# Kernel optimization log

Hardware: AMD Instinct MI355X
Metric: run time of the kernel (lower is better)

## Reference

```python
import jax, jax.numpy as jnp
import numpy as np

T = 2048          # total (flattened) tokens
HID = 4096
NQ = 32           # query heads
NKV = 8           # kv heads
D = 128           # head_dim
B = 4             # dllm block length (block-sparse attention block)
WIN = 1024        # sliding window
EPS = 1e-6


def _rope_tables():
    # standard RoPE cos/sin tables, half-dim frequencies duplicated
    inv_freq = 1.0 / (10000.0 ** (np.arange(0, D, 2, dtype=np.float32) / D))
    pos = np.arange(T, dtype=np.float32)
    freqs = np.outer(pos, inv_freq)                     # [T, D/2]
    emb = np.concatenate([freqs, freqs], axis=-1)       # [T, D]
    return jnp.asarray(np.cos(emb)), jnp.asarray(np.sin(emb))


def setup_inputs() -> dict:
    key = jax.random.key(0)
    ks = jax.random.split(key, 4)
    cos, sin = _rope_tables()
    return {
        "hidden_states": jax.random.normal(ks[0], (T, HID), jnp.float32),
        "cos": cos,
        "sin": sin,
        "w_qkv": jax.random.normal(ks[1], (HID, (NQ + 2 * NKV) * D), jnp.float32) * (HID ** -0.5),
        "q_norm_w": jnp.ones((D,), jnp.float32),
        "k_norm_w": jnp.ones((D,), jnp.float32),
        "w_o": jax.random.normal(ks[2], (NQ * D, HID), jnp.float32) * ((NQ * D) ** -0.5),
    }


def _rmsnorm(x, w):
    # per-head RMSNorm over last dim (head_dim)
    var = jnp.mean(jnp.square(x), axis=-1, keepdims=True)
    return x * jax.lax.rsqrt(var + EPS) * w


def _rotate_half(x):
    x1, x2 = jnp.split(x, 2, axis=-1)
    return jnp.concatenate([-x2, x1], axis=-1)


def reference(hidden_states, cos, sin, w_qkv, q_norm_w, k_norm_w, w_o):
    # fused QKV projection on flattened tokens [T, HID]
    qkv = hidden_states @ w_qkv                                  # [T, (NQ+2NKV)*D]
    q, k, v = jnp.split(qkv, [NQ * D, (NQ + NKV) * D], axis=-1)
    q = q.reshape(T, NQ, D)
    k = k.reshape(T, NKV, D)
    v = v.reshape(T, NKV, D)

    # per-head QK RMSNorm
    q = _rmsnorm(q, q_norm_w)
    k = _rmsnorm(k, k_norm_w)

    # RoPE
    c = cos[:, None, :]
    s = sin[:, None, :]
    q = q * c + _rotate_half(q) * s
    k = k * c + _rotate_half(k) * s

    # GQA: expand kv heads to query heads
    groups = NQ // NKV
    k = jnp.repeat(k, groups, axis=1)                            # [T, NQ, D]
    v = jnp.repeat(v, groups, axis=1)

    # block-sparse (dLLM block-causal) + sliding-window mask:
    # token q attends to token j iff block(j) <= block(q) (full bidirectional
    # attention within a dllm block, causal across blocks) AND j is within
    # the sliding window.
    pos = jnp.arange(T)
    qb = pos // B
    allowed = (qb[None, :] <= qb[:, None]) & ((pos[:, None] - pos[None, :]) < WIN)

    scale = D ** -0.5
    scores = jnp.einsum("qhd,khd->hqk", q, k) * scale            # [NQ, T, T]
    scores = jnp.where(allowed[None, :, :], scores, jnp.float32(-1e30))
    probs = jax.nn.softmax(scores, axis=-1)
    attn = jnp.einsum("hqk,khd->qhd", probs, v)                   # [T, NQ, D]

    out = attn.reshape(T, NQ * D) @ w_o                           # [T, HID]
    return out
```

## Files before the change

kernel.cpp:

```cpp
#include <hip/hip_runtime.h>
#include <hip/hip_bf16.h>

typedef unsigned short u16;
typedef __attribute__((ext_vector_type(8))) short bf16x8;
typedef __attribute__((ext_vector_type(4))) float f32x4;
typedef __attribute__((ext_vector_type(8))) u16 u16x8;
typedef __attribute__((ext_vector_type(4))) u16 u16x4;

#define T_SEQ 2048
#define HID 4096
#define NQ 32
#define NKV 8
#define DH 128
#define WIN 1024

__device__ __forceinline__ u16 f2bf(float f) {
  union { float f; unsigned int u; } v; v.f = f;
  unsigned int u = v.u;
  unsigned int r = (u + 0x7FFFu + ((u >> 16) & 1u)) >> 16;
  return (u16)r;
}
__device__ __forceinline__ float bf2f(u16 b) {
  union { unsigned int u; float f; } v; v.u = ((unsigned int)b) << 16;
  return v.f;
}

__device__ __forceinline__ void gload16(const void* g, void* l) {
  __builtin_amdgcn_global_load_lds(
      (const __attribute__((address_space(1))) unsigned int*)g,
      (__attribute__((address_space(3))) unsigned int*)l, 16, 0, 0);
}

__global__ __launch_bounds__(256) void f32_to_bf16(const float* __restrict__ in,
                                                   u16* __restrict__ out, int n) {
  int i = (blockIdx.x * 256 + threadIdx.x) * 8;
  if (i >= n) return;
  float4 a = *(const float4*)(in + i);
  float4 b = *(const float4*)(in + i + 4);
  u16x8 r;
  r[0] = f2bf(a.x); r[1] = f2bf(a.y); r[2] = f2bf(a.z); r[3] = f2bf(a.w);
  r[4] = f2bf(b.x); r[5] = f2bf(b.y); r[6] = f2bf(b.z); r[7] = f2bf(b.w);
  *(u16x8*)(out + i) = r;
}

__global__ __launch_bounds__(256) void transpose_f32_to_bf16(const float* __restrict__ in,
                                                             u16* __restrict__ out,
                                                             int R, int C) {
  __shared__ float tile[64][65];
  int c0 = blockIdx.x * 64, r0 = blockIdx.y * 64;
  int tx = threadIdx.x, ty = threadIdx.y;
#pragma unroll
  for (int i = 0; i < 64; i += 16) {
    float4 v = *(const float4*)(in + (size_t)(r0 + ty + i) * C + c0 + tx * 4);
    tile[ty + i][tx * 4 + 0] = v.x;
    tile[ty + i][tx * 4 + 1] = v.y;
    tile[ty + i][tx * 4 + 2] = v.z;
    tile[ty + i][tx * 4 + 3] = v.w;
  }
  __syncthreads();
#pragma unroll
  for (int i = 0; i < 64; i += 16) {
    u16x4 o;
#pragma unroll
    for (int j = 0; j < 4; ++j) o[j] = f2bf(tile[tx * 4 + j][ty + i]);
    *(u16x4*)(out + (size_t)(c0 + ty + i) * R + r0 + tx * 4) = o;
  }
}

template <int NF, bool BF16OUT>
__global__ __launch_bounds__(512, 2) void gemm_2w(const u16* __restrict__ A,
                                                  const u16* __restrict__ Bt,
                                                  void* __restrict__ Cv,
                                                  int N, int K, int NT) {
  constexpr int HN = NF * 16;
  constexpr int BN = 4 * HN;
  constexpr int NB = BN / 64;
  __shared__ u16 lsA[2][16384];
  __shared__ u16 lsB[2][BN * 64];
  const int tid = threadIdx.x;
  const int lane = tid & 63, w = tid >> 6;
  const int wm = w >> 1, wn = w & 1;
  const int l15 = lane & 15, l4 = lane >> 4;

  const int nwg = gridDim.x;
  const int cpx = nwg >> 3;
  const int bid = blockIdx.x;
  const int swz = (bid & 7) * cpx + (bid >> 3);
  const int bm = (swz & 7) * 256;
  const int bn = (swz >> 3) * BN;

  auto stageA = [&](int unit, int slot, int kt) {
    int r = tid >> 3, cp = tid & 7;
    int scp = cp ^ (r & 7);
    gload16(A + (size_t)(bm + unit * 64 + r) * K + kt * 64 + scp * 8,
            (char*)lsA[slot] + (unit * 512 + tid) * 16);
  };
  auto stageB = [&](int unit, int slot, int kt) {
    int r = tid >> 3, cp = tid & 7;
    int scp = cp ^ (r & 7);
    gload16(Bt + (size_t)(bn + unit * 64 + r) * K + kt * 64 + scp * 8,
            (char*)lsB[slot] + (unit * 512 + tid) * 16);
  };
  auto rdA = [&](int slot, int mh, int mf, int ks) -> bf16x8 {
    int r = wm * 64 + mh * 32 + mf * 16 + l15;
    int ch = (ks * 4 + l4) ^ (r & 7);
    return *(const bf16x8*)(lsA[slot] + r * 64 + ch * 8);
  };
  auto rdB = [&](int slot, int nh, int nf, int ks) -> bf16x8 {
    int r = wn * 2 * HN + nh * HN + nf * 16 + l15;
    int ch = (ks * 4 + l4) ^ (r & 7);
    return *(const bf16x8*)(lsB[slot] + r * 64 + ch * 8);
  };

#define WAIT_NB() do { if constexpr (NB == 3) asm volatile("s_waitcnt vmcnt(3)" ::: "memory"); \
                       else                   asm volatile("s_waitcnt vmcnt(2)" ::: "memory"); } while (0)

  f32x4 acc[4][2 * NF] = {};
  bf16x8 afA[2][2], afB[2][2], bfr[2 * NF][2];

  stageA(0, 0, 0); stageA(1, 0, 0); stageA(2, 0, 0); stageA(3, 0, 0);
#pragma unroll
  for (int u = 0; u < NB; ++u) stageB(u, 0, 0);
#pragma unroll
  for (int u = 0; u < NB; ++u) stageB(u, 1, 1);
  WAIT_NB();
  __builtin_amdgcn_s_barrier();

  for (int t = 0; t < NT; ++t) {
    const int s = t & 1;
    const int ktA = (t + 1 < NT) ? t + 1 : NT - 1;
    const int ktB = (t + 2 < NT) ? t + 2 : NT - 1;

#pragma unroll
    for (int mf = 0; mf < 2; ++mf)
#pragma unroll
      for (int ks = 0; ks < 2; ++ks) afA[mf][ks] = rdA(s, 0, mf, ks);
#pragma unroll
    for (int nf = 0; nf < NF; ++nf)
#pragma unroll
      for (int ks = 0; ks < 2; ++ks) {
        bfr[nf][ks] = rdB(s, 0, nf, ks);
        bfr[NF + nf][ks] = rdB(s, 1, nf, ks);
      }
    stageA(0, s ^ 1, ktA); stageA(1, s ^ 1, ktA);
    stageA(2, s ^ 1, ktA); stageA(3, s ^ 1, ktA);
    __builtin_amdgcn_s_barrier();
    asm volatile("s_waitcnt lgkmcnt(0)" ::: "memory");
    __builtin_amdgcn_sched_barrier(0);
    __builtin_amdgcn_s_setprio(1);
#pragma unroll
    for (int mf = 0; mf < 2; ++mf)
#pragma unroll
      for (int nf = 0; nf < 2 * NF; ++nf) {
        acc[mf][nf] = __builtin_amdgcn_mfma_f32_16x16x32_bf16(afA[mf][0], bfr[nf][0], acc[mf][nf], 0, 0, 0);
        acc[mf][nf] = __builtin_amdgcn_mfma_f32_16x16x32_bf16(afA[mf][1], bfr[nf][1], acc[mf][nf], 0, 0, 0);
      }
    __builtin_amdgcn_s_setprio(0);
    __builtin_amdgcn_s_barrier();

#pragma unroll
    for (int mf = 0; mf < 2; ++mf)
#pragma unroll
      for (int ks = 0; ks < 2; ++ks) afB[mf][ks] = rdA(s, 1, mf, ks);
#pragma unroll
    for (int u = 0; u < NB; ++u) stageB(u, s, ktB);
    __builtin_amdgcn_s_barrier();
    asm volatile("s_waitcnt lgkmcnt(0)" ::: "memory");
    __builtin_amdgcn_sched_barrier(0);
    __builtin_amdgcn_s_setprio(1);
#pragma unroll
    for (int mf = 0; mf < 2; ++mf)
#pragma unroll
      for (int nf = 0; nf < 2 * NF; ++nf) {
        acc[2 + mf][nf] = __builtin_amdgcn_mfma_f32_16x16x32_bf16(afB[mf][0], bfr[nf][0], acc[2 + mf][nf], 0, 0, 0);
        acc[2 + mf][nf] = __builtin_amdgcn_mfma_f32_16x16x32_bf16(afB[mf][1], bfr[nf][1], acc[2 + mf][nf], 0, 0, 0);
      }
    __builtin_amdgcn_s_setprio(0);
    WAIT_NB();
    __builtin_amdgcn_s_barrier();
  }

  asm volatile("s_waitcnt vmcnt(0)" ::: "memory");

#pragma unroll
  for (int mi = 0; mi < 4; ++mi)
#pragma unroll
    for (int ni = 0; ni < 2 * NF; ++ni) {
      int row = bm + wm * 64 + mi * 16 + l4 * 4;
      int col = bn + wn * 2 * HN + ni * 16 + l15;
      if constexpr (BF16OUT) {
        u16* dst = (u16*)Cv;
#pragma unroll
        for (int j = 0; j < 4; ++j)
          dst[(size_t)(row + j) * N + col] = f2bf(acc[mi][ni][j]);
      } else {
        float* p = (float*)Cv + (size_t)row * N + col;
        p[0] = acc[mi][ni][0];
        p[(size_t)N] = acc[mi][ni][1];
        p[2 * (size_t)N] = acc[mi][ni][2];
        p[3 * (size_t)N] = acc[mi][ni][3];
      }
    }
#undef WAIT_NB
}

__global__ __launch_bounds__(256) void rope_kernel(const u16* __restrict__ qkv,
                                                   const float* __restrict__ cosb,
                                                   const float* __restrict__ sinb,
                                                   const float* __restrict__ qw,
                                                   const float* __restrict__ kw,
                                                   u16* __restrict__ Qo,
                                                   u16* __restrict__ Ko,
                                                   u16* __restrict__ Vt) {
  int wid = threadIdx.x >> 6, lane = threadIdx.x & 63;
  int item = blockIdx.x * 4 + wid;
  int t = item / 48, hid = item % 48;
  const u16* x = qkv + (size_t)t * 6144 + hid * 128;
  float x1 = bf2f(x[lane]), x2 = bf2f(x[lane + 64]);
  if (hid < NQ + NKV) {
    float ss = x1 * x1 + x2 * x2;
    for (int off = 32; off; off >>= 1) ss += __shfl_xor(ss, off);
    float inv = rsqrtf(ss * (1.0f / 128.0f) + 1e-6f);
    const float* wn = (hid < NQ) ? qw : kw;
    float n1 = x1 * inv * wn[lane], n2 = x2 * inv * wn[lane + 64];
    float c1 = cosb[t * 128 + lane], s1 = sinb[t * 128 + lane];
    float c2 = cosb[t * 128 + lane + 64], s2 = sinb[t * 128 + lane + 64];
    float o1 = n1 * c1 - n2 * s1;
    float o2 = n2 * c2 + n1 * s2;
    if (hid < NQ) {
      const float scale = 0.08838834764831845f;
      u16* q = Qo + ((size_t)hid * T_SEQ + t) * 128;
      q[lane] = f2bf(o1 * scale); q[lane + 64] = f2bf(o2 * scale);
    } else {
      int h = hid - NQ;
      u16* k = Ko + ((size_t)h * T_SEQ + t) * 128;
      k[lane] = f2bf(o1); k[lane + 64] = f2bf(o2);
    }
  } else {
    int h = hid - (NQ + NKV);
    Vt[((size_t)h * 128 + lane) * T_SEQ + t] = x[lane];
    Vt[((size_t)h * 128 + lane + 64) * T_SEQ + t] = x[lane + 64];
  }
}

__global__ __launch_bounds__(256) void attn_kernel(const u16* __restrict__ Q,
                                                   const u16* __restrict__ Kb,
                                                   const u16* __restrict__ Vt,
                                                   u16* __restrict__ O) {
  __shared__ u16 kls[2][64 * 128];
  __shared__ u16 vls[2][128 * 64];
  __shared__ u16 plds[4][16 * 72];

  const int tid = threadIdx.x;
  const int lane = tid & 63, w = tid >> 6;
  const int l15 = lane & 15, l4 = lane >> 4;
  const int h = blockIdx.x;
  const int q0 = blockIdx.y * 64;
  const int wq0 = q0 + w * 16;
  const int kvh = h >> 2;

  bf16x8 qf[4];
  {
    const u16* qrow = Q + ((size_t)h * T_SEQ + (wq0 + l15)) * DH;
    for (int ks = 0; ks < 4; ++ks)
      qf[ks] = *(const bf16x8*)(qrow + ks * 32 + l4 * 8);
  }

  f32x4 acc[8] = {};
  float m = -1e30f, lsum = 0.f;

  int ks0 = q0 - (WIN - 1); if (ks0 < 0) ks0 = 0;
  ks0 &= ~63;
  const int kend = q0;

  auto stage = [&](int b, int k0) {
#pragma unroll
    for (int c = 0; c < 4; ++c) {
      int base = w * 4096 + c * 1024;
      int idx = base / 16 + lane;
      {
        int row = idx >> 4;
        int col = (idx & 15) ^ (row & 7);
        gload16(Kb + ((size_t)kvh * T_SEQ + k0 + row) * DH + col * 8,
                (char*)kls[b] + base);
      }
      {
        int d = idx >> 3;
        int ch = (idx & 7) ^ (d & 7);
        gload16(Vt + ((size_t)kvh * DH + d) * T_SEQ + k0 + ch * 8,
                (char*)vls[b] + base);
      }
    }
  };

  stage(0, ks0);
  int buf = 0;
  for (int k0 = ks0; k0 <= kend; k0 += 64) {
    bool more = (k0 + 64 <= kend);
    if (more) stage(buf ^ 1, k0 + 64);
    if (more) { asm volatile("s_waitcnt vmcnt(8)" ::: "memory"); }
    else      { asm volatile("s_waitcnt vmcnt(0)" ::: "memory"); }
    __builtin_amdgcn_s_barrier();
    __builtin_amdgcn_sched_barrier(0);

    if (k0 <= wq0 + 15 && k0 + 63 >= wq0 - (WIN - 1)) {
      f32x4 st[4];
      __builtin_amdgcn_s_setprio(1);
#pragma unroll
      for (int kh = 0; kh < 4; ++kh) {
        f32x4 s = {};
        int row = kh * 16 + l15;
        const char* kb = (const char*)kls[buf] + row * 256;
#pragma unroll
        for (int ks = 0; ks < 4; ++ks) {
          int chunk = (ks * 4 + l4) ^ (row & 7);
          bf16x8 kf = *(const bf16x8*)(kb + chunk * 16);
          s = __builtin_amdgcn_mfma_f32_16x16x32_bf16(kf, qf[ks], s, 0, 0, 0);
        }
        st[kh] = s;
      }
      __builtin_amdgcn_s_setprio(0);
      const int q = wq0 + l15;
      float pv[4][4];
      float mx = -3e38f;
      if (k0 + 64 <= wq0 && k0 >= wq0 - 1008) {
#pragma unroll
        for (int kh = 0; kh < 4; ++kh)
#pragma unroll
          for (int i = 0; i < 4; ++i) {
            pv[kh][i] = st[kh][i];
            mx = fmaxf(mx, pv[kh][i]);
          }
      } else {
#pragma unroll
        for (int kh = 0; kh < 4; ++kh)
#pragma unroll
          for (int i = 0; i < 4; ++i) {
            int k = k0 + kh * 16 + l4 * 4 + i;
            bool ok = ((k >> 2) <= (q >> 2)) && (q - k < WIN);
            float s = ok ? st[kh][i] : -3e38f;
            pv[kh][i] = s;
            mx = fmaxf(mx, s);
          }
      }
      mx = fmaxf(mx, __shfl_xor(mx, 16));
      mx = fmaxf(mx, __shfl_xor(mx, 32));
      if (!__all(mx <= m + 8.f)) {
        float mn = fmaxf(m, mx);
        float sc = __expf(m - mn);
        m = mn;
        lsum *= sc;
#pragma unroll
        for (int nt = 0; nt < 8; ++nt)
#pragma unroll
          for (int i = 0; i < 4; ++i) acc[nt][i] *= sc;
      }
      float rs = 0.f;
#pragma unroll
      for (int kh = 0; kh < 4; ++kh)
#pragma unroll
        for (int i = 0; i < 4; ++i) {
          float p = __expf(pv[kh][i] - m);
          pv[kh][i] = p;
          rs += p;
        }
      rs += __shfl_xor(rs, 16);
      rs += __shfl_xor(rs, 32);
      lsum += rs;
      u16* pw = plds[w];
#pragma unroll
      for (int kh = 0; kh < 4; ++kh) {
        unsigned int d0 = (unsigned int)f2bf(pv[kh][0]) | ((unsigned int)f2bf(pv[kh][1]) << 16);
        unsigned int d1 = (unsigned int)f2bf(pv[kh][2]) | ((unsigned int)f2bf(pv[kh][3]) << 16);
        *(unsigned int*)(pw + l15 * 72 + kh * 16 + l4 * 4) = d0;
        *(unsigned int*)(pw + l15 * 72 + kh * 16 + l4 * 4 + 2) = d1;
      }
      bf16x8 pf0 = *(const bf16x8*)(pw + l15 * 72 + l4 * 8);
      bf16x8 pf1 = *(const bf16x8*)(pw + l15 * 72 + 32 + l4 * 8);
      __builtin_amdgcn_s_setprio(1);
#pragma unroll
      for (int nt = 0; nt < 8; ++nt) {
        int d = nt * 16 + l15;
        int ch0 = l4 ^ (d & 7);
        int ch1 = (4 + l4) ^ (d & 7);
        bf16x8 vf0 = *(const bf16x8*)((const char*)vls[buf] + d * 128 + ch0 * 16);
        bf16x8 vf1 = *(const bf16x8*)((const char*)vls[buf] + d * 128 + ch1 * 16);
        acc[nt] = __builtin_amdgcn_mfma_f32_16x16x32_bf16(vf0, pf0, acc[nt], 0, 0, 0);
        acc[nt] = __builtin_amdgcn_mfma_f32_16x16x32_bf16(vf1, pf1, acc[nt], 0, 0, 0);
      }
      __builtin_amdgcn_s_setprio(0);
    }
    __builtin_amdgcn_sched_barrier(0);
    __builtin_amdgcn_s_barrier();
    buf ^= 1;
  }

  float inv = 1.0f / lsum;
#pragma unroll
  for (int nt = 0; nt < 8; ++nt) {
    u16x4 o;
#pragma unroll
    for (int i = 0; i < 4; ++i) o[i] = f2bf(acc[nt][i] * inv);
    *(u16x4*)(O + (size_t)(wq0 + l15) * (NQ * DH) + h * DH + nt * 16 + l4 * 4) = o;
  }
}

extern "C" void kernel_launch(void* const* d_in, const int* in_sizes, int n_in,
                              void* d_out, int out_size, void* d_ws, size_t ws_size,
                              hipStream_t stream) {
  const float* hidden = (const float*)d_in[0];
  const float* cosb   = (const float*)d_in[1];
  const float* sinb   = (const float*)d_in[2];
  const float* w_qkv  = (const float*)d_in[3];
  const float* qnw    = (const float*)d_in[4];
  const float* knw    = (const float*)d_in[5];
  const float* w_o    = (const float*)d_in[6];
  float* out = (float*)d_out;
  char* ws = (char*)d_ws;

  u16*   wqkvT  = (u16*)(ws);
  u16*   hid_bf = (u16*)(ws + ((size_t)48 << 20));
  u16*   qkv_bf = (u16*)(ws + ((size_t)64 << 20));
  u16*   q_bf   = (u16*)(ws + ((size_t)112 << 20));
  u16*   k_bf   = (u16*)(ws + ((size_t)128 << 20));
  u16*   vt_bf  = (u16*)(ws + ((size_t)132 << 20));
  u16*   attn_bf= (u16*)(ws + ((size_t)48 << 20));
  u16*   woT    = (u16*)(ws);

  f32_to_bf16<<<4096, 256, 0, stream>>>(hidden, hid_bf, T_SEQ * HID);
  transpose_f32_to_bf16<<<dim3(96, 64), dim3(16, 16), 0, stream>>>(w_qkv, wqkvT, HID, 6144);
  gemm_2w<3, true><<<256, 512, 0, stream>>>(hid_bf, wqkvT, qkv_bf, 6144, HID, 64);
  transpose_f32_to_bf16<<<dim3(64, 64), dim3(16, 16), 0, stream>>>(w_o, woT, NQ * DH, HID);
  rope_kernel<<<(T_SEQ * 48) / 4, 256, 0, stream>>>(qkv_bf, cosb, sinb, qnw, knw, q_bf, k_bf, vt_bf);
  attn_kernel<<<dim3(NQ, T_SEQ / 64), 256, 0, stream>>>(q_bf, k_bf, vt_bf, attn_bf);
  gemm_2w<2, false><<<256, 512, 0, stream>>>(attn_bf, woT, out, HID, NQ * DH, 64);
}
```

Before: 319.9 us.

## Add software-pipelined output-projection GEMM with triple-buffered A and swizzled LDS

Replaces the generic output-projection GEMM with a dedicated kernel that triple-buffers A tiles and double-buffers B tiles in LDS, using XOR-swizzled layouts and explicit waitcnt/barrier placement. Each k-tile is split into two half-phases so register fragment loads for the next step overlap the current MFMA work, with s_setprio raising priority during MFMA bursts. It also remaps workgroup IDs for L2 locality. The hand-scheduled synchronization adds complexity and risks LDS pressure limiting occupancy.

```diff
diff --git a/kernel.cpp b/kernel.cpp
--- a/kernel.cpp
+++ b/kernel.cpp
@@ -202,6 +202,138 @@
       }
     }
 #undef WAIT_NB
+}
+
+#define MFMA16(a, b, c) __builtin_amdgcn_mfma_f32_16x16x32_bf16(a, b, c, 0, 0, 0)
+__global__ __launch_bounds__(512, 2) void gemm2_p(const u16* __restrict__ A,
+                                                  const u16* __restrict__ Bt,
+                                                  float* __restrict__ C,
+                                                  int N, int K, int NT) {
+  __shared__ u16 lsA[3][16384];
+  __shared__ u16 lsB[2][8192];
+  const int tid = threadIdx.x;
+  const int lane = tid & 63, w = tid >> 6;
+  const int wm = w >> 1, wn = w & 1;
+  const int l15 = lane & 15, l4 = lane >> 4;
+
+  const int nwg = gridDim.x;
+  const int cpx = nwg >> 3;
+  const int bid = blockIdx.x;
+  const int swz = (bid & 7) * cpx + (bid >> 3);
+  const int bm = (swz & 7) * 256;
+  const int bn = (swz >> 3) * 128;
+
+  auto stageA = [&](int unit, int slot, int kt) {
+    int r = tid >> 3, cp = tid & 7;
+    int scp = cp ^ (r & 7);
+    gload16(A + (size_t)(bm + unit * 64 + r) * K + kt * 64 + scp * 8,
+            (char*)lsA[slot] + (unit * 512 + tid) * 16);
+  };
+  auto stageB = [&](int unit, int slot, int kt) {
+    int r = tid >> 3, cp = tid & 7;
+    int scp = cp ^ (r & 7);
+    gload16(Bt + (size_t)(bn + unit * 64 + r) * K + kt * 64 + scp * 8,
+            (char*)lsB[slot] + (unit * 512 + tid) * 16);
+  };
+  auto rdA = [&](int slot, int mfi, int ks) -> bf16x8 {
+    int r = wm * 64 + mfi * 16 + l15;
+    int ch = (ks * 4 + l4) ^ (r & 7);
+    return *(const bf16x8*)(lsA[slot] + r * 64 + ch * 8);
+  };
+  auto rdB = [&](int slot, int nf, int ks) -> bf16x8 {
+    int r = wn * 64 + nf * 16 + l15;
+    int ch = (ks * 4 + l4) ^ (r & 7);
+    return *(const bf16x8*)(lsB[slot] + r * 64 + ch * 8);
+  };
+
+  f32x4 acc[4][4] = {};
+  bf16x8 afA0[4], afA1[4], bfr0_[8], bfr1_[8], afB[4];
+
+  stageA(0, 0, 0); stageA(1, 0, 0); stageA(2, 0, 0); stageA(3, 0, 0);
+  stageB(0, 0, 0); stageB(1, 0, 0);
+  stageA(0, 1, 1); stageA(1, 1, 1); stageA(2, 1, 1); stageA(3, 1, 1);
+  stageB(0, 1, 1); stageB(1, 1, 1);
+  asm volatile("s_waitcnt vmcnt(6)" ::: "memory");
+  __builtin_amdgcn_s_barrier();
+#pragma unroll
+  for (int mf = 0; mf < 2; ++mf)
+#pragma unroll
+    for (int ks = 0; ks < 2; ++ks) afA0[mf * 2 + ks] = rdA(0, mf, ks);
+#pragma unroll
+  for (int nf = 0; nf < 4; ++nf)
+#pragma unroll
+    for (int ks = 0; ks < 2; ++ks) bfr0_[nf * 2 + ks] = rdB(0, nf, ks);
+  asm volatile("s_waitcnt lgkmcnt(0)" ::: "memory");
+  __builtin_amdgcn_sched_barrier(0);
+
+#define TILE_P(T, AFC, BFC, AFN, BFN) {                                        \
+    const int s3 = (T) % 3, s3n = ((T) + 1) % 3, s3s = ((T) + 2) % 3;          \
+    const int s2 = (T) & 1, s2n = ((T) + 1) & 1;                               \
+    const int ktt = ((T) + 2 < NT) ? (T) + 2 : NT - 1;                         \
+                                                             \
+    stageA(0, s3s, ktt); stageA(1, s3s, ktt);                                  \
+    stageA(2, s3s, ktt); stageA(3, s3s, ktt);                                  \
+    asm volatile("s_waitcnt vmcnt(4)" ::: "memory");                           \
+    _Pragma("unroll")                                                          \
+    for (int mf = 0; mf < 2; ++mf)                                             \
+      _Pragma("unroll")                                                        \
+      for (int ks = 0; ks < 2; ++ks) afB[mf * 2 + ks] = rdA(s3, 2 + mf, ks);   \
+    _Pragma("unroll")                                                          \
+    for (int nf = 0; nf < 4; ++nf)                                             \
+      _Pragma("unroll")                                                        \
+      for (int ks = 0; ks < 2; ++ks) BFN[nf * 2 + ks] = rdB(s2n, nf, ks);      \
+    __builtin_amdgcn_s_setprio(1);                                             \
+    _Pragma("unroll")                                                          \
+    for (int mf = 0; mf < 2; ++mf)                                             \
+      _Pragma("unroll")                                                        \
+      for (int nf = 0; nf < 4; ++nf) {                                         \
+        acc[mf][nf] = MFMA16(AFC[mf * 2 + 0], BFC[nf * 2 + 0], acc[mf][nf]);   \
+        acc[mf][nf] = MFMA16(AFC[mf * 2 + 1], BFC[nf * 2 + 1], acc[mf][nf]);   \
+      }                                                                        \
+    __builtin_amdgcn_s_setprio(0);                                             \
+    asm volatile("s_waitcnt lgkmcnt(0)" ::: "memory");                         \
+    __builtin_amdgcn_sched_barrier(0);                                         \
+    __builtin_amdgcn_s_barrier();                                              \
+                                                             \
+    _Pragma("unroll")                                                          \
+    for (int mf = 0; mf < 2; ++mf)                                             \
+      _Pragma("unroll")                                                        \
+      for (int ks = 0; ks < 2; ++ks) AFN[mf * 2 + ks] = rdA(s3n, mf, ks);      \
+    stageB(0, s2, ktt); stageB(1, s2, ktt);                                    \
+    __builtin_amdgcn_s_setprio(1);                                             \
+    _Pragma("unroll")                                                          \
+    for (int mf = 0; mf < 2; ++mf)                                             \
+      _Pragma("unroll")                                                        \
+      for (int nf = 0; nf < 4; ++nf) {                                         \
+        acc[2 + mf][nf] = MFMA16(afB[mf * 2 + 0], BFC[nf * 2 + 0], acc[2 + mf][nf]); \
+        acc[2 + mf][nf] = MFMA16(afB[mf * 2 + 1], BFC[nf * 2 + 1], acc[2 + mf][nf]); \
+      }                                                                        \
+    __builtin_amdgcn_s_setprio(0);                                             \
+    asm volatile("s_waitcnt lgkmcnt(0)" ::: "memory");                         \
+    __builtin_amdgcn_sched_barrier(0);                                         \
+    __builtin_amdgcn_s_barrier();                                              \
+  }
+
+  for (int t = 0; t < NT; t += 2) {
+    TILE_P(t, afA0, bfr0_, afA1, bfr1_);
+    TILE_P(t + 1, afA1, bfr1_, afA0, bfr0_);
+  }
+#undef TILE_P
+
+  asm volatile("s_waitcnt vmcnt(0)" ::: "memory");
+
+#pragma unroll
+  for (int mi = 0; mi < 4; ++mi)
+#pragma unroll
+    for (int ni = 0; ni < 4; ++ni) {
+      int row = bm + wm * 64 + mi * 16 + l4 * 4;
+      int col = bn + wn * 64 + ni * 16 + l15;
+      float* p = C + (size_t)row * N + col;
+      p[0] = acc[mi][ni][0];
+      p[(size_t)N] = acc[mi][ni][1];
+      p[2 * (size_t)N] = acc[mi][ni][2];
+      p[3 * (size_t)N] = acc[mi][ni][3];
+    }
 }
 
 __global__ __launch_bounds__(256) void rope_kernel(const u16* __restrict__ qkv,
@@ -433,5 +565,5 @@
   transpose_f32_to_bf16<<<dim3(64, 64), dim3(16, 16), 0, stream>>>(w_o, woT, NQ * DH, HID);
   rope_kernel<<<(T_SEQ * 48) / 4, 256, 0, stream>>>(qkv_bf, cosb, sinb, qnw, knw, q_bf, k_bf, vt_bf);
   attn_kernel<<<dim3(NQ, T_SEQ / 64), 256, 0, stream>>>(q_bf, k_bf, vt_bf, attn_bf);
-  gemm_2w<2, false><<<256, 512, 0, stream>>>(attn_bf, woT, out, HID, NQ * DH, 64);
-}
+  gemm2_p<<<256, 512, 0, stream>>>(attn_bf, woT, out, HID, NQ * DH, 64);
+}
```

New measurement: 330.7 us. 3.4% more time.

## Add triple-buffered A-tile GEMM variant for QKV projection

Applied to the files above, without the earlier changes.

Adds a gemm_3s kernel that keeps three LDS slots for the A tile (B stays double-buffered) and prefetches two k-steps ahead, splitting each iteration into two MFMA halves with staged loads between them. It is used for the QKV projection GEMM in place of gemm_2w. The aim is to hide more global-load latency behind the matrix math. In exchange it uses more shared memory, which may limit occupancy at 2 workgroups per CU, and its vmcnt accounting is hand-tuned.

```diff
diff --git a/kernel.cpp b/kernel.cpp
--- a/kernel.cpp
+++ b/kernel.cpp
@@ -65,6 +65,145 @@
     for (int j = 0; j < 4; ++j) o[j] = f2bf(tile[tx * 4 + j][ty + i]);
     *(u16x4*)(out + (size_t)(c0 + ty + i) * R + r0 + tx * 4) = o;
   }
+}
+
+template <int NF, bool BF16OUT>
+__global__ __launch_bounds__(512, 2) void gemm_3s(const u16* __restrict__ A,
+                                                  const u16* __restrict__ Bt,
+                                                  void* __restrict__ Cv,
+                                                  int N, int K, int NT) {
+  constexpr int HN = NF * 16;
+  constexpr int BN = 4 * HN;
+  constexpr int NB = BN / 64;
+  __shared__ u16 lsA[3][16384];
+  __shared__ u16 lsB[2][BN * 64];
+  const int tid = threadIdx.x;
+  const int lane = tid & 63, w = tid >> 6;
+  const int wm = w >> 1, wn = w & 1;
+  const int l15 = lane & 15, l4 = lane >> 4;
+
+  const int nwg = gridDim.x;
+  const int cpx = nwg >> 3;
+  const int bid = blockIdx.x;
+  const int swz = (bid & 7) * cpx + (bid >> 3);
+  const int bm = (swz & 7) * 256;
+  const int bn = (swz >> 3) * BN;
+
+  auto stageA = [&](int unit, int slot, int kt) {
+    int r = tid >> 3, cp = tid & 7;
+    int scp = cp ^ (r & 7);
+    gload16(A + (size_t)(bm + unit * 64 + r) * K + kt * 64 + scp * 8,
+            (char*)lsA[slot] + (unit * 512 + tid) * 16);
+  };
+  auto stageB = [&](int unit, int slot, int kt) {
+    int r = tid >> 3, cp = tid & 7;
+    int scp = cp ^ (r & 7);
+    gload16(Bt + (size_t)(bn + unit * 64 + r) * K + kt * 64 + scp * 8,
+            (char*)lsB[slot] + (unit * 512 + tid) * 16);
+  };
+  auto rdA = [&](int slot, int mh, int mf, int ks) -> bf16x8 {
+    int r = wm * 64 + mh * 32 + mf * 16 + l15;
+    int ch = (ks * 4 + l4) ^ (r & 7);
+    return *(const bf16x8*)(lsA[slot] + r * 64 + ch * 8);
+  };
+  auto rdB = [&](int slot, int nh, int nf, int ks) -> bf16x8 {
+    int r = wn * 2 * HN + nh * HN + nf * 16 + l15;
+    int ch = (ks * 4 + l4) ^ (r & 7);
+    return *(const bf16x8*)(lsB[slot] + r * 64 + ch * 8);
+  };
+
+#define WAIT_AB() do { if constexpr (NB == 3) asm volatile("s_waitcnt vmcnt(7)" ::: "memory"); \
+                       else                   asm volatile("s_waitcnt vmcnt(6)" ::: "memory"); } while (0)
+
+  f32x4 acc[4][2 * NF] = {};
+  bf16x8 afA[2][2], afB[2][2], bfr[2 * NF][2];
+
+  stageA(0, 0, 0); stageA(1, 0, 0); stageA(2, 0, 0); stageA(3, 0, 0);
+#pragma unroll
+  for (int u = 0; u < NB; ++u) stageB(u, 0, 0);
+  stageA(0, 1, 1); stageA(1, 1, 1); stageA(2, 1, 1); stageA(3, 1, 1);
+#pragma unroll
+  for (int u = 0; u < NB; ++u) stageB(u, 1, 1);
+  WAIT_AB();
+  __builtin_amdgcn_s_barrier();
+
+  for (int t = 0; t < NT; ++t) {
+    const int s3 = t % 3;
+    const int s3s = (t + 2) % 3;
+    const int s2 = t & 1;
+    const int ktt = (t + 2 < NT) ? t + 2 : NT - 1;
+
+#pragma unroll
+    for (int mf = 0; mf < 2; ++mf)
+#pragma unroll
+      for (int ks = 0; ks < 2; ++ks) afA[mf][ks] = rdA(s3, 0, mf, ks);
+#pragma unroll
+    for (int nf = 0; nf < NF; ++nf)
+#pragma unroll
+      for (int ks = 0; ks < 2; ++ks) {
+        bfr[nf][ks] = rdB(s2, 0, nf, ks);
+        bfr[NF + nf][ks] = rdB(s2, 1, nf, ks);
+      }
+    stageA(0, s3s, ktt); stageA(1, s3s, ktt);
+    stageA(2, s3s, ktt); stageA(3, s3s, ktt);
+    __builtin_amdgcn_s_barrier();
+    asm volatile("s_waitcnt lgkmcnt(0)" ::: "memory");
+    __builtin_amdgcn_sched_barrier(0);
+    __builtin_amdgcn_s_setprio(1);
+#pragma unroll
+    for (int mf = 0; mf < 2; ++mf)
+#pragma unroll
+      for (int nf = 0; nf < 2 * NF; ++nf) {
+        acc[mf][nf] = __builtin_amdgcn_mfma_f32_16x16x32_bf16(afA[mf][0], bfr[nf][0], acc[mf][nf], 0, 0, 0);
+        acc[mf][nf] = __builtin_amdgcn_mfma_f32_16x16x32_bf16(afA[mf][1], bfr[nf][1], acc[mf][nf], 0, 0, 0);
+      }
+    __builtin_amdgcn_s_setprio(0);
+    __builtin_amdgcn_s_barrier();
+
+#pragma unroll
+    for (int mf = 0; mf < 2; ++mf)
+#pragma unroll
+      for (int ks = 0; ks < 2; ++ks) afB[mf][ks] = rdA(s3, 1, mf, ks);
+#pragma unroll
+    for (int u = 0; u < NB; ++u) stageB(u, s2, ktt);
+    __builtin_amdgcn_s_barrier();
+    asm volatile("s_waitcnt lgkmcnt(0)" ::: "memory");
+    __builtin_amdgcn_sched_barrier(0);
+    __builtin_amdgcn_s_setprio(1);
+#pragma unroll
+    for (int mf = 0; mf < 2; ++mf)
+#pragma unroll
+      for (int nf = 0; nf < 2 * NF; ++nf) {
+        acc[2 + mf][nf] = __builtin_amdgcn_mfma_f32_16x16x32_bf16(afB[mf][0], bfr[nf][0], acc[2 + mf][nf], 0, 0, 0);
+        acc[2 + mf][nf] = __builtin_amdgcn_mfma_f32_16x16x32_bf16(afB[mf][1], bfr[nf][1], acc[2 + mf][nf], 0, 0, 0);
+      }
+    __builtin_amdgcn_s_setprio(0);
+    WAIT_AB();
+    __builtin_amdgcn_s_barrier();
+  }
+
+  asm volatile("s_waitcnt vmcnt(0)" ::: "memory");
+
+#pragma unroll
+  for (int mi = 0; mi < 4; ++mi)
+#pragma unroll
+    for (int ni = 0; ni < 2 * NF; ++ni) {
+      int row = bm + wm * 64 + mi * 16 + l4 * 4;
+      int col = bn + wn * 2 * HN + ni * 16 + l15;
+      if constexpr (BF16OUT) {
+        u16* dst = (u16*)Cv;
+#pragma unroll
+        for (int j = 0; j < 4; ++j)
+          dst[(size_t)(row + j) * N + col] = f2bf(acc[mi][ni][j]);
+      } else {
+        float* p = (float*)Cv + (size_t)row * N + col;
+        p[0] = acc[mi][ni][0];
+        p[(size_t)N] = acc[mi][ni][1];
+        p[2 * (size_t)N] = acc[mi][ni][2];
+        p[3 * (size_t)N] = acc[mi][ni][3];
+      }
+    }
+#undef WAIT_AB
 }
 
 template <int NF, bool BF16OUT>
@@ -429,7 +568,7 @@
 
   f32_to_bf16<<<4096, 256, 0, stream>>>(hidden, hid_bf, T_SEQ * HID);
   transpose_f32_to_bf16<<<dim3(96, 64), dim3(16, 16), 0, stream>>>(w_qkv, wqkvT, HID, 6144);
-  gemm_2w<3, true><<<256, 512, 0, stream>>>(hid_bf, wqkvT, qkv_bf, 6144, HID, 64);
+  gemm_3s<3, true><<<256, 512, 0, stream>>>(hid_bf, wqkvT, qkv_bf, 6144, HID, 64);
   transpose_f32_to_bf16<<<dim3(64, 64), dim3(16, 16), 0, stream>>>(w_o, woT, NQ * DH, HID);
   rope_kernel<<<(T_SEQ * 48) / 4, 256, 0, stream>>>(qkv_bf, cosb, sinb, qnw, knw, q_bf, k_bf, vt_bf);
   attn_kernel<<<dim3(NQ, T_SEQ / 64), 256, 0, stream>>>(q_bf, k_bf, vt_bf, attn_bf);
```

After: 319.1 us. Within noise of the previous version (-0.2%).

## Merge GEMM half-steps into one phase with triple-buffered B; coalesce V transpose

Applied to the files above, without the earlier changes.

The GEMM main loop used to be split into two half-steps, each with its own barriers. It now runs one phase per K-tile: all A and B fragments are read at once and the next A and B tiles are issued together. B gets a third LDS slot so its prefetch two tiles ahead cannot overwrite data still being read, which removes two barriers per iteration. Separately, the rope kernel now writes V row-major with contiguous stores, and a new tiled LDS transpose kernel produces the V-transposed layout instead of scattered strided stores. The cost is more LDS per GEMM block, more live fragment registers, and one extra kernel launch plus a round trip of V through memory.

```diff
diff --git a/kernel.cpp b/kernel.cpp
--- a/kernel.cpp
+++ b/kernel.cpp
@@ -67,8 +67,31 @@
   }
 }
 
+__global__ __launch_bounds__(256) void v_transpose(const u16* __restrict__ Vn,
+                                                   u16* __restrict__ Vt) {
+  __shared__ u16 tile[64][68];
+  int tx = threadIdx.x & 15, ty = threadIdx.x >> 4;
+  int t0 = blockIdx.x * 64, dh0 = blockIdx.y * 64;
+#pragma unroll
+  for (int i = 0; i < 64; i += 16) {
+    u16x4 v = *(const u16x4*)(Vn + (size_t)(t0 + ty + i) * 1024 + dh0 + tx * 4);
+    tile[ty + i][tx * 4 + 0] = v[0];
+    tile[ty + i][tx * 4 + 1] = v[1];
+    tile[ty + i][tx * 4 + 2] = v[2];
+    tile[ty + i][tx * 4 + 3] = v[3];
+  }
+  __syncthreads();
+#pragma unroll
+  for (int i = 0; i < 64; i += 16) {
+    u16x4 o;
+#pragma unroll
+    for (int j = 0; j < 4; ++j) o[j] = tile[tx * 4 + j][ty + i];
+    *(u16x4*)(Vt + (size_t)(dh0 + ty + i) * 2048 + t0 + tx * 4) = o;
+  }
+}
+
 template <int NF, bool BF16OUT>
-__global__ __launch_bounds__(512, 2) void gemm_2w(const u16* __restrict__ A,
+__global__ __launch_bounds__(512, 2) void gemm_1w(const u16* __restrict__ A,
                                                   const u16* __restrict__ Bt,
                                                   void* __restrict__ Cv,
                                                   int N, int K, int NT) {
@@ -76,7 +99,7 @@
   constexpr int BN = 4 * HN;
   constexpr int NB = BN / 64;
   __shared__ u16 lsA[2][16384];
-  __shared__ u16 lsB[2][BN * 64];
+  __shared__ u16 lsB[3][BN * 64];
   const int tid = threadIdx.x;
   const int lane = tid & 63, w = tid >> 6;
   const int wm = w >> 1, wn = w & 1;
@@ -101,13 +124,13 @@
     gload16(Bt + (size_t)(bn + unit * 64 + r) * K + kt * 64 + scp * 8,
             (char*)lsB[slot] + (unit * 512 + tid) * 16);
   };
-  auto rdA = [&](int slot, int mh, int mf, int ks) -> bf16x8 {
-    int r = wm * 64 + mh * 32 + mf * 16 + l15;
+  auto rdA = [&](int slot, int mf, int ks) -> bf16x8 {
+    int r = wm * 64 + mf * 16 + l15;
     int ch = (ks * 4 + l4) ^ (r & 7);
     return *(const bf16x8*)(lsA[slot] + r * 64 + ch * 8);
   };
-  auto rdB = [&](int slot, int nh, int nf, int ks) -> bf16x8 {
-    int r = wn * 2 * HN + nh * HN + nf * 16 + l15;
+  auto rdB = [&](int slot, int nf, int ks) -> bf16x8 {
+    int r = wn * 2 * HN + nf * 16 + l15;
     int ch = (ks * 4 + l4) ^ (r & 7);
     return *(const bf16x8*)(lsB[slot] + r * 64 + ch * 8);
   };
@@ -116,7 +139,7 @@
                        else                   asm volatile("s_waitcnt vmcnt(2)" ::: "memory"); } while (0)
 
   f32x4 acc[4][2 * NF] = {};
-  bf16x8 afA[2][2], afB[2][2], bfr[2 * NF][2];
+  bf16x8 afA[4][2], bfr[2 * NF][2];
 
   stageA(0, 0, 0); stageA(1, 0, 0); stageA(2, 0, 0); stageA(3, 0, 0);
 #pragma unroll
@@ -127,53 +150,31 @@
   __builtin_amdgcn_s_barrier();
 
   for (int t = 0; t < NT; ++t) {
-    const int s = t & 1;
+    const int sA = t & 1, sB = t % 3;
     const int ktA = (t + 1 < NT) ? t + 1 : NT - 1;
     const int ktB = (t + 2 < NT) ? t + 2 : NT - 1;
 
 #pragma unroll
-    for (int mf = 0; mf < 2; ++mf)
-#pragma unroll
-      for (int ks = 0; ks < 2; ++ks) afA[mf][ks] = rdA(s, 0, mf, ks);
-#pragma unroll
-    for (int nf = 0; nf < NF; ++nf)
-#pragma unroll
-      for (int ks = 0; ks < 2; ++ks) {
-        bfr[nf][ks] = rdB(s, 0, nf, ks);
-        bfr[NF + nf][ks] = rdB(s, 1, nf, ks);
-      }
-    stageA(0, s ^ 1, ktA); stageA(1, s ^ 1, ktA);
-    stageA(2, s ^ 1, ktA); stageA(3, s ^ 1, ktA);
-    __builtin_amdgcn_s_barrier();
+    for (int mf = 0; mf < 4; ++mf)
+#pragma unroll
+      for (int ks = 0; ks < 2; ++ks) afA[mf][ks] = rdA(sA, mf, ks);
+#pragma unroll
+    for (int nf = 0; nf < 2 * NF; ++nf)
+#pragma unroll
+      for (int ks = 0; ks < 2; ++ks) bfr[nf][ks] = rdB(sB, nf, ks);
+    stageA(0, (t + 1) & 1, ktA); stageA(1, (t + 1) & 1, ktA);
+    stageA(2, (t + 1) & 1, ktA); stageA(3, (t + 1) & 1, ktA);
+#pragma unroll
+    for (int u = 0; u < NB; ++u) stageB(u, (t + 2) % 3, ktB);
     asm volatile("s_waitcnt lgkmcnt(0)" ::: "memory");
     __builtin_amdgcn_sched_barrier(0);
     __builtin_amdgcn_s_setprio(1);
 #pragma unroll
-    for (int mf = 0; mf < 2; ++mf)
+    for (int mf = 0; mf < 4; ++mf)
 #pragma unroll
       for (int nf = 0; nf < 2 * NF; ++nf) {
         acc[mf][nf] = __builtin_amdgcn_mfma_f32_16x16x32_bf16(afA[mf][0], bfr[nf][0], acc[mf][nf], 0, 0, 0);
         acc[mf][nf] = __builtin_amdgcn_mfma_f32_16x16x32_bf16(afA[mf][1], bfr[nf][1], acc[mf][nf], 0, 0, 0);
-      }
-    __builtin_amdgcn_s_setprio(0);
-    __builtin_amdgcn_s_barrier();
-
-#pragma unroll
-    for (int mf = 0; mf < 2; ++mf)
-#pragma unroll
-      for (int ks = 0; ks < 2; ++ks) afB[mf][ks] = rdA(s, 1, mf, ks);
-#pragma unroll
-    for (int u = 0; u < NB; ++u) stageB(u, s, ktB);
-    __builtin_amdgcn_s_barrier();
-    asm volatile("s_waitcnt lgkmcnt(0)" ::: "memory");
-    __builtin_amdgcn_sched_barrier(0);
-    __builtin_amdgcn_s_setprio(1);
-#pragma unroll
-    for (int mf = 0; mf < 2; ++mf)
-#pragma unroll
-      for (int nf = 0; nf < 2 * NF; ++nf) {
-        acc[2 + mf][nf] = __builtin_amdgcn_mfma_f32_16x16x32_bf16(afB[mf][0], bfr[nf][0], acc[2 + mf][nf], 0, 0, 0);
-        acc[2 + mf][nf] = __builtin_amdgcn_mfma_f32_16x16x32_bf16(afB[mf][1], bfr[nf][1], acc[2 + mf][nf], 0, 0, 0);
       }
     __builtin_amdgcn_s_setprio(0);
     WAIT_NB();
@@ -211,7 +212,7 @@
                                                    const float* __restrict__ kw,
                                                    u16* __restrict__ Qo,
                                                    u16* __restrict__ Ko,
-                                                   u16* __restrict__ Vt) {
+                                                   u16* __restrict__ Vn) {
   int wid = threadIdx.x >> 6, lane = threadIdx.x & 63;
   int item = blockIdx.x * 4 + wid;
   int t = item / 48, hid = item % 48;
@@ -238,8 +239,9 @@
     }
   } else {
     int h = hid - (NQ + NKV);
-    Vt[((size_t)h * 128 + lane) * T_SEQ + t] = x[lane];
-    Vt[((size_t)h * 128 + lane + 64) * T_SEQ + t] = x[lane + 64];
+    u16* vn = Vn + (size_t)t * 1024 + h * 128;
+    vn[lane] = x[lane];
+    vn[lane + 64] = x[lane + 64];
   }
 }
 
@@ -421,6 +423,7 @@
   u16*   wqkvT  = (u16*)(ws);
   u16*   hid_bf = (u16*)(ws + ((size_t)48 << 20));
   u16*   qkv_bf = (u16*)(ws + ((size_t)64 << 20));
+  u16*   vn_bf  = (u16*)(ws + ((size_t)88 << 20));
   u16*   q_bf   = (u16*)(ws + ((size_t)112 << 20));
   u16*   k_bf   = (u16*)(ws + ((size_t)128 << 20));
   u16*   vt_bf  = (u16*)(ws + ((size_t)132 << 20));
@@ -429,9 +432,10 @@
 
   f32_to_bf16<<<4096, 256, 0, stream>>>(hidden, hid_bf, T_SEQ * HID);
   transpose_f32_to_bf16<<<dim3(96, 64), dim3(16, 16), 0, stream>>>(w_qkv, wqkvT, HID, 6144);
-  gemm_2w<3, true><<<256, 512, 0, stream>>>(hid_bf, wqkvT, qkv_bf, 6144, HID, 64);
+  gemm_1w<3, true><<<256, 512, 0, stream>>>(hid_bf, wqkvT, qkv_bf, 6144, HID, 64);
   transpose_f32_to_bf16<<<dim3(64, 64), dim3(16, 16), 0, stream>>>(w_o, woT, NQ * DH, HID);
-  rope_kernel<<<(T_SEQ * 48) / 4, 256, 0, stream>>>(qkv_bf, cosb, sinb, qnw, knw, q_bf, k_bf, vt_bf);
+  rope_kernel<<<(T_SEQ * 48) / 4, 256, 0, stream>>>(qkv_bf, cosb, sinb, qnw, knw, q_bf, k_bf, vn_bf);
+  v_transpose<<<dim3(32, 16), 256, 0, stream>>>(vn_bf, vt_bf);
   attn_kernel<<<dim3(NQ, T_SEQ / 64), 256, 0, stream>>>(q_bf, k_bf, vt_bf, attn_bf);
-  gemm_2w<2, false><<<256, 512, 0, stream>>>(attn_bf, woT, out, HID, NQ * DH, 64);
-}
+  gemm_1w<2, false><<<256, 512, 0, stream>>>(attn_bf, woT, out, HID, NQ * DH, 64);
+}
```

Measured after the change: 311.5 us. 2.6% less time.
